# Performance work log

Measured on AMD Instinct MI355X. Metric: run time of the kernel, lower is better.

The kernel has to match this reference:

```python
import jax, jax.numpy as jnp
import numpy as np

H = 512          # hidden_size
SF = 4           # scale_factor
B, S, L = 16, 2048, 2

def setup_inputs() -> dict:
    key = jax.random.key(0)
    ks = jax.random.split(key, 9)
    return {
        "hidden": jax.random.normal(ks[0], (L, B, H * SF), dtype=jnp.float32),
        "encoder_outputs": jax.random.normal(ks[1], (B, S, H * SF), dtype=jnp.float32),
        "We": jax.random.normal(ks[2], (H, H * SF), dtype=jnp.float32) * 0.02,
        "be": jax.random.normal(ks[3], (H,), dtype=jnp.float32) * 0.02,
        "Wh": jax.random.normal(ks[4], (H, H * SF), dtype=jnp.float32) * 0.02,
        "bh": jax.random.normal(ks[5], (H,), dtype=jnp.float32) * 0.02,
        "Wa": jax.random.normal(ks[6], (H, 2 * H), dtype=jnp.float32) * 0.02,
        "ba": jax.random.normal(ks[7], (H,), dtype=jnp.float32) * 0.02,
        "v": jax.random.uniform(ks[8], (1, H), dtype=jnp.float32),
    }

def reference(hidden, encoder_outputs, We, be, Wh, bh, Wa, ba, v):
    # hidden[-1]: [B, 4H] -> [B, H]
    h = hidden[-1] @ Wh.T + bh
    # encoder_outputs: [B, S, 4H] -> [B, S, H]
    eo = jnp.einsum('bsf,hf->bsh', encoder_outputs, We) + be
    # concat([h broadcast to S, eo]) @ Wa.T == h @ Wa_h.T + eo @ Wa_e.T (split concat matmul)
    Wa_h, Wa_e = Wa[:, :H], Wa[:, H:]
    energy = jnp.tanh(h[:, None, :] @ Wa_h.T + jnp.einsum('bsh,kh->bsk', eo, Wa_e) + ba)  # [B,S,H]
    scores = jnp.einsum('bsh,h->bs', energy, v[0])           # [B,S]
    attn_weights = jax.nn.softmax(scores, axis=1)            # [B,S]
    context_vector = jnp.einsum('bs,bsh->bh', attn_weights, eo)  # [B,H]
    return (context_vector, attn_weights)
```

## Files before the change

kernel.cpp:

```cpp
#include <hip/hip_runtime.h>
#include <math.h>

#define HH 512
#define FF 2048
#define BB 16
#define SS 2048
#define MM 32768

using f32x4 = __attribute__((ext_vector_type(4))) float;
using s16x8 = __attribute__((ext_vector_type(8))) short;

struct __align__(8)  US4 { unsigned short x, y, z, w; };
struct __align__(16) US8 { unsigned short s[8]; };

__device__ __forceinline__ unsigned short f2bf(float f) {
  unsigned int u = __builtin_bit_cast(unsigned int, f);
  u += 0x7fffu + ((u >> 16) & 1u);
  return (unsigned short)(u >> 16);
}
__device__ __forceinline__ float bf2f(unsigned short u) {
  unsigned int x = ((unsigned int)u) << 16;
  return __builtin_bit_cast(float, x);
}
__device__ __forceinline__ void gload_lds16(const void* g, void* l) {
  __builtin_amdgcn_global_load_lds(
      (const __attribute__((address_space(1))) unsigned int*)g,
      (__attribute__((address_space(3))) unsigned int*)l, 16, 0, 0);
}

__global__ void k_conv(const float* __restrict__ We, const float* __restrict__ Wa,
                       unsigned short* __restrict__ OWe, unsigned short* __restrict__ OWa) {
  int bid = blockIdx.x, t = threadIdx.x;
  if (bid < 1024) {
    int idx = bid * 256 + t;
    f32x4 x = *(const f32x4*)(We + (size_t)idx * 4);
    US4 p{f2bf(x.x), f2bf(x.y), f2bf(x.z), f2bf(x.w)};
    *(US4*)(OWe + (size_t)idx * 4) = p;
  } else {
    int idx = (bid - 1024) * 256 + t;
    int k = idx >> 7, h4 = idx & 127;
    f32x4 x = *(const f32x4*)(Wa + (size_t)k * 1024 + 512 + h4 * 4);
    US4 p{f2bf(x.x), f2bf(x.y), f2bf(x.z), f2bf(x.w)};
    *(US4*)(OWa + (size_t)idx * 4) = p;
  }
}

__global__ void k_h(const float* __restrict__ hidden, const float* __restrict__ Wh,
                    const float* __restrict__ bh, float* __restrict__ h_ws) {
  int t = threadIdx.x, lane = t & 63, wid = t >> 6;
  int out = blockIdx.x * 4 + wid;
  int b = out >> 9, j = out & 511;
  const float* hr = hidden + (1) * BB * FF + b * FF;
  const float* wr = Wh + (size_t)j * FF;
  float a = 0.f;
#pragma unroll
  for (int i = 0; i < 8; ++i) {
    int o = i * 256 + lane * 4;
    f32x4 x = *(const f32x4*)(hr + o);
    f32x4 y = *(const f32x4*)(wr + o);
    a += x.x * y.x + x.y * y.y + x.z * y.z + x.w * y.w;
  }
#pragma unroll
  for (int m = 32; m; m >>= 1) a += __shfl_xor(a, m);
  if (lane == 0) h_ws[out] = a + bh[j];
}

__global__ void k_bb(const float* __restrict__ h_ws, const float* __restrict__ Wa,
                     const float* __restrict__ ba, float* __restrict__ bb_ws) {
  int t = threadIdx.x, lane = t & 63, wid = t >> 6;
  int out = blockIdx.x * 4 + wid;
  int b = out >> 9, k = out & 511;
  const float* hr = h_ws + b * HH;
  const float* wa = Wa + (size_t)k * 1024;
  float a = 0.f;
#pragma unroll
  for (int i = 0; i < 2; ++i) {
    int o = i * 256 + lane * 4;
    f32x4 x = *(const f32x4*)(hr + o);
    f32x4 y = *(const f32x4*)(wa + o);
    a += x.x * y.x + x.y * y.y + x.z * y.z + x.w * y.w;
  }
#pragma unroll
  for (int m = 32; m; m >>= 1) a += __shfl_xor(a, m);
  if (lane == 0) bb_ws[out] = a + ba[k];
}

__global__ __launch_bounds__(512, 4) void k_gemm1f(
    const float* __restrict__ enc, const unsigned short* __restrict__ Web,
    const float* __restrict__ be, const unsigned short* __restrict__ Waeb,
    const float* __restrict__ bbw, const float* __restrict__ vv,
    unsigned short* __restrict__ eo, float* __restrict__ sp) {
  __shared__ unsigned short smem[36864];
  unsigned short* As = smem;
  unsigned short* Bs = smem + 4096;
  const int t = threadIdx.x, lane = t & 63, wid = t >> 6;
  const int m0 = blockIdx.x * 64;
  const float* enc_m0 = enc + (size_t)m0 * FF;
  f32x4 acc[4][4] = {};

  f32x4 areg[2];
#pragma unroll
  for (int i = 0; i < 2; ++i) {
    int idx = i * 512 + t, row = idx >> 4, c4 = idx & 15;
    areg[i] = *(const f32x4*)(enc_m0 + (size_t)row * FF + c4 * 4);
  }

#pragma unroll 1
  for (int kt = 0; kt < FF; kt += 64) {
#pragma unroll
    for (int i = 0; i < 8; ++i) {
      int idx = i * 512 + t, row = idx >> 3, c = idx & 7, sc = c ^ (row & 7);
      gload_lds16(Web + (size_t)row * FF + kt + sc * 8, Bs + idx * 8);
    }
#pragma unroll
    for (int i = 0; i < 2; ++i) {
      int idx = i * 512 + t, row = idx >> 4, c4 = idx & 15;
      f32x4 x = areg[i];
      US4 p{f2bf(x.x), f2bf(x.y), f2bf(x.z), f2bf(x.w)};
      int byte = row * 128 + ((c4 * 8) ^ ((row & 7) << 4));
      *(US4*)((char*)As + byte) = p;
    }
    {
      int ktn = (kt + 64 < FF) ? kt + 64 : 0;
#pragma unroll
      for (int i = 0; i < 2; ++i) {
        int idx = i * 512 + t, row = idx >> 4, c4 = idx & 15;
        areg[i] = *(const f32x4*)(enc_m0 + (size_t)row * FF + ktn + c4 * 4);
      }
    }
    asm volatile("s_waitcnt vmcnt(2) lgkmcnt(0)" ::: "memory");
    __builtin_amdgcn_s_barrier();
    __builtin_amdgcn_sched_barrier(0);
#pragma unroll
    for (int ks = 0; ks < 2; ++ks) {
      s16x8 af[4], bfr[4];
#pragma unroll
      for (int mi = 0; mi < 4; ++mi) {
        int row = mi * 16 + (lane & 15);
        int byte = row * 128 + (((ks * 64) + (lane >> 4) * 16) ^ ((row & 7) << 4));
        af[mi] = *(const s16x8*)((const char*)As + byte);
      }
#pragma unroll
      for (int ni = 0; ni < 4; ++ni) {
        int row = wid * 64 + ni * 16 + (lane & 15);
        int byte = row * 128 + (((ks * 64) + (lane >> 4) * 16) ^ ((row & 7) << 4));
        bfr[ni] = *(const s16x8*)((const char*)Bs + byte);
      }
#pragma unroll
      for (int mi = 0; mi < 4; ++mi)
#pragma unroll
        for (int ni = 0; ni < 4; ++ni)
          acc[mi][ni] = __builtin_amdgcn_mfma_f32_16x16x32_bf16(af[mi], bfr[ni], acc[mi][ni], 0, 0, 0);
    }
    asm volatile("s_waitcnt lgkmcnt(0)" ::: "memory");
    __builtin_amdgcn_s_barrier();
    __builtin_amdgcn_sched_barrier(0);
  }

  unsigned short* Cs = smem + 4096;
#pragma unroll
  for (int ni = 0; ni < 4; ++ni) {
    int col = wid * 64 + ni * 16 + (lane & 15);
    float bev = be[col];
#pragma unroll
    for (int mi = 0; mi < 4; ++mi)
#pragma unroll
      for (int j = 0; j < 4; ++j) {
        int row = mi * 16 + (lane >> 4) * 4 + j;
        int byte = row * 1024 + ((col * 2) ^ ((row & 7) << 4));
        *(unsigned short*)((char*)Cs + byte) = f2bf(acc[mi][ni][j] + bev);
      }
  }
  __syncthreads();

#pragma unroll
  for (int i = 0; i < 8; ++i) {
    int idx = i * 512 + t, row = idx >> 6, c = idx & 63;
    int byte = row * 1024 + ((c * 16) ^ ((row & 7) << 4));
    *(US8*)(eo + (size_t)(m0 + row) * HH + c * 8) = *(const US8*)((const char*)Cs + byte);
  }

  f32x4 acc2[4][4] = {};
#pragma unroll
  for (int kt2 = 0; kt2 < HH; kt2 += 64) {
#pragma unroll
    for (int ks = 0; ks < 2; ++ks) {
      int k2 = kt2 + ks * 32 + (lane >> 4) * 8;
      s16x8 af[4], bfr[4];
#pragma unroll
      for (int mi = 0; mi < 4; ++mi) {
        int row = mi * 16 + (lane & 15);
        int byte = row * 1024 + ((k2 * 2) ^ ((row & 7) << 4));
        af[mi] = *(const s16x8*)((const char*)Cs + byte);
      }
#pragma unroll
      for (int ni = 0; ni < 4; ++ni) {
        int nrow = wid * 64 + ni * 16 + (lane & 15);
        bfr[ni] = *(const s16x8*)(Waeb + (size_t)nrow * HH + k2);
      }
#pragma unroll
      for (int mi = 0; mi < 4; ++mi)
#pragma unroll
        for (int ni = 0; ni < 4; ++ni)
          acc2[mi][ni] = __builtin_amdgcn_mfma_f32_16x16x32_bf16(af[mi], bfr[ni], acc2[mi][ni], 0, 0, 0);
    }
  }

  const int b = m0 >> 11;
  float vcol[4], bcol[4];
#pragma unroll
  for (int ni = 0; ni < 4; ++ni) {
    int col = wid * 64 + ni * 16 + (lane & 15);
    vcol[ni] = vv[col];
    bcol[ni] = bbw[b * HH + col];
  }
  float ps[4][4];
#pragma unroll
  for (int mi = 0; mi < 4; ++mi)
#pragma unroll
    for (int j = 0; j < 4; ++j) {
      float s = 0.f;
#pragma unroll
      for (int ni = 0; ni < 4; ++ni)
        s += tanhf(acc2[mi][ni][j] + bcol[ni]) * vcol[ni];
      ps[mi][j] = s;
    }
#pragma unroll
  for (int m = 1; m < 16; m <<= 1)
#pragma unroll
    for (int mi = 0; mi < 4; ++mi)
#pragma unroll
      for (int j = 0; j < 4; ++j) ps[mi][j] += __shfl_xor(ps[mi][j], m);
  float* red = (float*)smem;
  if ((lane & 15) == 0) {
#pragma unroll
    for (int mi = 0; mi < 4; ++mi)
#pragma unroll
      for (int j = 0; j < 4; ++j)
        red[wid * 64 + mi * 16 + (lane >> 4) * 4 + j] = ps[mi][j];
  }
  __syncthreads();
  if (t < 64) {
    float s = 0.f;
#pragma unroll
    for (int w = 0; w < 8; ++w) s += red[w * 64 + t];
    sp[m0 + t] = s;
  }
}

__global__ void k_softmax(const float* __restrict__ sp, float* __restrict__ attn) {
  const int b = blockIdx.x, t = threadIdx.x, lane = t & 63, wid = t >> 6;
  __shared__ float red[4];
  float vals[8], lmax = -3.0e38f;
#pragma unroll
  for (int i = 0; i < 8; ++i) {
    float x = sp[b * SS + t + i * 256];
    vals[i] = x;
    lmax = fmaxf(lmax, x);
  }
#pragma unroll
  for (int m = 32; m; m >>= 1) lmax = fmaxf(lmax, __shfl_xor(lmax, m));
  if (lane == 0) red[wid] = lmax;
  __syncthreads();
  lmax = fmaxf(fmaxf(red[0], red[1]), fmaxf(red[2], red[3]));
  __syncthreads();
  float lsum = 0.f;
#pragma unroll
  for (int i = 0; i < 8; ++i) {
    vals[i] = __expf(vals[i] - lmax);
    lsum += vals[i];
  }
#pragma unroll
  for (int m = 32; m; m >>= 1) lsum += __shfl_xor(lsum, m);
  if (lane == 0) red[wid] = lsum;
  __syncthreads();
  float inv = 1.0f / (red[0] + red[1] + red[2] + red[3]);
#pragma unroll
  for (int i = 0; i < 8; ++i) attn[b * SS + t + i * 256] = vals[i] * inv;
}

__global__ __launch_bounds__(512) void k_ctx1(const unsigned short* __restrict__ eo,
                                              const float* __restrict__ attn,
                                              float* __restrict__ cp) {
  __shared__ float red[8][512];
  const int b = blockIdx.x >> 4, ch = blockIdx.x & 15, t = threadIdx.x;
  const int tg = t & 63, sg = t >> 6;
  const float* aw = attn + b * SS + ch * 128;
  float acc[8] = {};
#pragma unroll 4
  for (int i = 0; i < 16; ++i) {
    int s = sg + i * 8;
    float w = aw[s];
    US8 vv8 = *(const US8*)(eo + (size_t)(b * SS + ch * 128 + s) * HH + tg * 8);
#pragma unroll
    for (int j = 0; j < 8; ++j) acc[j] += w * bf2f(vv8.s[j]);
  }
#pragma unroll
  for (int j = 0; j < 8; ++j) red[sg][tg * 8 + j] = acc[j];
  __syncthreads();
  float a = 0.f;
#pragma unroll
  for (int g = 0; g < 8; ++g) a += red[g][t];
  cp[(size_t)blockIdx.x * HH + t] = a;
}

__global__ void k_ctx2(const float* __restrict__ cp, float* __restrict__ ctx) {
  const int b = blockIdx.x, h = threadIdx.x;
  float a = 0.f;
#pragma unroll
  for (int c = 0; c < 16; ++c) a += cp[(size_t)(b * 16 + c) * HH + h];
  ctx[b * HH + h] = a;
}

extern "C" void kernel_launch(void* const* d_in, const int* in_sizes, int n_in,
                              void* d_out, int out_size, void* d_ws, size_t ws_size,
                              hipStream_t stream) {
  (void)in_sizes; (void)n_in; (void)out_size; (void)ws_size;
  const float* hidden = (const float*)d_in[0];
  const float* enc    = (const float*)d_in[1];
  const float* We     = (const float*)d_in[2];
  const float* be     = (const float*)d_in[3];
  const float* Wh     = (const float*)d_in[4];
  const float* bh     = (const float*)d_in[5];
  const float* Wa     = (const float*)d_in[6];
  const float* ba     = (const float*)d_in[7];
  const float* v      = (const float*)d_in[8];

  float* out  = (float*)d_out;
  float* ctx  = out;
  float* attn = out + BB * HH;

  char* ws = (char*)d_ws;
  unsigned short* Web  = (unsigned short*)ws;  ws += (size_t)HH * FF * 2;
  unsigned short* Waeb = (unsigned short*)ws;  ws += (size_t)HH * HH * 2;
  float* h_ws  = (float*)ws;                   ws += (size_t)BB * HH * 4;
  float* bb_ws = (float*)ws;                   ws += (size_t)BB * HH * 4;
  unsigned short* eo = (unsigned short*)ws;    ws += (size_t)MM * HH * 2;
  float* sp = (float*)ws;                      ws += (size_t)MM * 4;
  float* cp = (float*)ws;                      ws += (size_t)BB * 16 * HH * 4;

  k_conv<<<1280, 256, 0, stream>>>(We, Wa, Web, Waeb);
  k_h<<<2048, 256, 0, stream>>>(hidden, Wh, bh, h_ws);
  k_bb<<<2048, 256, 0, stream>>>(h_ws, Wa, ba, bb_ws);
  k_gemm1f<<<512, 512, 0, stream>>>(enc, Web, be, Waeb, bb_ws, v, eo, sp);
  k_softmax<<<16, 256, 0, stream>>>(sp, attn);
  k_ctx1<<<256, 512, 0, stream>>>(eo, attn, cp);
  k_ctx2<<<16, 512, 0, stream>>>(cp, ctx);
}
```

Measured before the change: 170.5 us.

## Load GEMM1 B fragments directly to registers and double-buffer A tile in LDS

The main encoder GEMM kernel no longer stages the bf16 weight tile through LDS with global_load_lds. Each wave now loads its B fragments straight from global memory into registers, ping-ponging between two register sets across the two k-halves. The fp32 activation tile is converted and written into a double-buffered LDS A tile, so each iteration needs one barrier and less LDS traffic. The cost is more VGPR pressure, uncoalesced per-lane global B loads that rely on L2 reuse across blocks, and a larger shared allocation that may lower occupancy.

```diff
diff --git a/kernel.cpp b/kernel.cpp
--- a/kernel.cpp
+++ b/kernel.cpp
@@ -21,11 +21,6 @@
 __device__ __forceinline__ float bf2f(unsigned short u) {
   unsigned int x = ((unsigned int)u) << 16;
   return __builtin_bit_cast(float, x);
-}
-__device__ __forceinline__ void gload_lds16(const void* g, void* l) {
-  __builtin_amdgcn_global_load_lds(
-      (const __attribute__((address_space(1))) unsigned int*)g,
-      (__attribute__((address_space(3))) unsigned int*)l, 16, 0, 0);
 }
 
 __global__ void k_conv(const float* __restrict__ We, const float* __restrict__ Wa,
@@ -90,74 +85,81 @@
     const float* __restrict__ be, const unsigned short* __restrict__ Waeb,
     const float* __restrict__ bbw, const float* __restrict__ vv,
     unsigned short* __restrict__ eo, float* __restrict__ sp) {
-  __shared__ unsigned short smem[36864];
-  unsigned short* As = smem;
-  unsigned short* Bs = smem + 4096;
+  __shared__ char smem[81920];
   const int t = threadIdx.x, lane = t & 63, wid = t >> 6;
   const int m0 = blockIdx.x * 64;
   const float* enc_m0 = enc + (size_t)m0 * FF;
   f32x4 acc[4][4] = {};
 
-  f32x4 areg[2];
-#pragma unroll
-  for (int i = 0; i < 2; ++i) {
-    int idx = i * 512 + t, row = idx >> 4, c4 = idx & 15;
-    areg[i] = *(const f32x4*)(enc_m0 + (size_t)row * FF + c4 * 4);
-  }
+  const int sRow = t & 63;
+  const int sKb  = t >> 6;
+  const int sDst = ((sKb * 4 + (sRow >> 4)) << 8) + ((sRow & 15) << 4);
+  const float* ap = enc_m0 + (size_t)sRow * FF + sKb * 8;
+
+  const unsigned short* bp = Web + (size_t)(wid * 64 + (lane & 15)) * FF + ((lane >> 4) << 3);
+
+  f32x4 ar0, ar1;
+  {
+    f32x4 w0 = *(const f32x4*)ap;
+    f32x4 w1 = *(const f32x4*)(ap + 4);
+    US8 o{f2bf(w0.x), f2bf(w0.y), f2bf(w0.z), f2bf(w0.w),
+          f2bf(w1.x), f2bf(w1.y), f2bf(w1.z), f2bf(w1.w)};
+    *(US8*)(smem + sDst) = o;
+    ar0 = *(const f32x4*)(ap + 64);
+    ar1 = *(const f32x4*)(ap + 68);
+  }
+  s16x8 bA[4], bB[4];
+#pragma unroll
+  for (int ni = 0; ni < 4; ++ni)
+    bA[ni] = *(const s16x8*)(bp + (size_t)ni * 16 * FF);
+  asm volatile("s_waitcnt lgkmcnt(0)" ::: "memory");
+  __builtin_amdgcn_s_barrier();
+  __builtin_amdgcn_sched_barrier(0);
 
 #pragma unroll 1
   for (int kt = 0; kt < FF; kt += 64) {
-#pragma unroll
-    for (int i = 0; i < 8; ++i) {
-      int idx = i * 512 + t, row = idx >> 3, c = idx & 7, sc = c ^ (row & 7);
-      gload_lds16(Web + (size_t)row * FF + kt + sc * 8, Bs + idx * 8);
-    }
-#pragma unroll
-    for (int i = 0; i < 2; ++i) {
-      int idx = i * 512 + t, row = idx >> 4, c4 = idx & 15;
-      f32x4 x = areg[i];
-      US4 p{f2bf(x.x), f2bf(x.y), f2bf(x.z), f2bf(x.w)};
-      int byte = row * 128 + ((c4 * 8) ^ ((row & 7) << 4));
-      *(US4*)((char*)As + byte) = p;
-    }
-    {
-      int ktn = (kt + 64 < FF) ? kt + 64 : 0;
-#pragma unroll
-      for (int i = 0; i < 2; ++i) {
-        int idx = i * 512 + t, row = idx >> 4, c4 = idx & 15;
-        areg[i] = *(const f32x4*)(enc_m0 + (size_t)row * FF + ktn + c4 * 4);
+    char* AsC = smem + (((kt >> 6) & 1) << 13);
+    char* AsN = smem + ((((kt >> 6) & 1) ^ 1) << 13);
+#pragma unroll
+    for (int ni = 0; ni < 4; ++ni)
+      bB[ni] = *(const s16x8*)(bp + (size_t)ni * 16 * FF + kt + 32);
+    if (kt < 1984) {
+      US8 o{f2bf(ar0.x), f2bf(ar0.y), f2bf(ar0.z), f2bf(ar0.w),
+            f2bf(ar1.x), f2bf(ar1.y), f2bf(ar1.z), f2bf(ar1.w)};
+      *(US8*)(AsN + sDst) = o;
+      if (kt < 1920) {
+        ar0 = *(const f32x4*)(ap + kt + 128);
+        ar1 = *(const f32x4*)(ap + kt + 132);
       }
     }
-    asm volatile("s_waitcnt vmcnt(2) lgkmcnt(0)" ::: "memory");
-    __builtin_amdgcn_s_barrier();
-    __builtin_amdgcn_sched_barrier(0);
-#pragma unroll
-    for (int ks = 0; ks < 2; ++ks) {
-      s16x8 af[4], bfr[4];
-#pragma unroll
-      for (int mi = 0; mi < 4; ++mi) {
-        int row = mi * 16 + (lane & 15);
-        int byte = row * 128 + (((ks * 64) + (lane >> 4) * 16) ^ ((row & 7) << 4));
-        af[mi] = *(const s16x8*)((const char*)As + byte);
-      }
-#pragma unroll
-      for (int ni = 0; ni < 4; ++ni) {
-        int row = wid * 64 + ni * 16 + (lane & 15);
-        int byte = row * 128 + (((ks * 64) + (lane >> 4) * 16) ^ ((row & 7) << 4));
-        bfr[ni] = *(const s16x8*)((const char*)Bs + byte);
-      }
-#pragma unroll
-      for (int mi = 0; mi < 4; ++mi)
-#pragma unroll
-        for (int ni = 0; ni < 4; ++ni)
-          acc[mi][ni] = __builtin_amdgcn_mfma_f32_16x16x32_bf16(af[mi], bfr[ni], acc[mi][ni], 0, 0, 0);
+    s16x8 af[4];
+#pragma unroll
+    for (int mi = 0; mi < 4; ++mi)
+      af[mi] = *(const s16x8*)(AsC + (((lane >> 4)) * 4 + mi) * 256 + ((lane & 15) << 4));
+#pragma unroll
+    for (int mi = 0; mi < 4; ++mi)
+#pragma unroll
+      for (int ni = 0; ni < 4; ++ni)
+        acc[mi][ni] = __builtin_amdgcn_mfma_f32_16x16x32_bf16(af[mi], bA[ni], acc[mi][ni], 0, 0, 0);
+    if (kt < 1984) {
+#pragma unroll
+      for (int ni = 0; ni < 4; ++ni)
+        bA[ni] = *(const s16x8*)(bp + (size_t)ni * 16 * FF + kt + 64);
     }
+#pragma unroll
+    for (int mi = 0; mi < 4; ++mi)
+      af[mi] = *(const s16x8*)(AsC + ((4 + (lane >> 4)) * 4 + mi) * 256 + ((lane & 15) << 4));
+#pragma unroll
+    for (int mi = 0; mi < 4; ++mi)
+#pragma unroll
+      for (int ni = 0; ni < 4; ++ni)
+        acc[mi][ni] = __builtin_amdgcn_mfma_f32_16x16x32_bf16(af[mi], bB[ni], acc[mi][ni], 0, 0, 0);
     asm volatile("s_waitcnt lgkmcnt(0)" ::: "memory");
     __builtin_amdgcn_s_barrier();
     __builtin_amdgcn_sched_barrier(0);
   }
 
-  unsigned short* Cs = smem + 4096;
+  unsigned short* Cs = (unsigned short*)(smem + 16384);
 #pragma unroll
   for (int ni = 0; ni < 4; ++ni) {
     int col = wid * 64 + ni * 16 + (lane & 15);
```

Result: slower. 243.7 us (+42.9%).

## Enlarge GEMM tile to 128 rows with double-buffered B in LDS

Applied to the files above, without the earlier changes.

The fused encoder GEMM kernel now processes 128 rows per block instead of 64. It double-buffers the We tile in LDS (a 144KB allocation) and lays A and B out in a fragment-friendly order without XOR swizzle. The K loop is unrolled two steps per iteration with register ping-pong for the fp32 A prefetch. The epilogue and second GEMM run in two 64-row halves. The aim is to halve the reloads of We per row of output and to overlap global loads with MFMA work, at the cost of one block per CU, only 256 blocks, and higher register pressure from 32 accumulators.

```diff
diff --git a/kernel.cpp b/kernel.cpp
--- a/kernel.cpp
+++ b/kernel.cpp
@@ -85,166 +85,215 @@
   if (lane == 0) bb_ws[out] = a + ba[k];
 }
 
-__global__ __launch_bounds__(512, 4) void k_gemm1f(
+template<int PAR, bool STB, bool LDA, bool WRA, int VM>
+__device__ __forceinline__ void stepB(
+    const float* apA, const float* apB, const unsigned short* Web, char* smem,
+    int kt, int t, int lane, int wid, int aDst0, int aDst1,
+    const int* bRow, const int* bKb,
+    f32x4& l0, f32x4& l1, f32x4& l2, f32x4& l3,
+    const f32x4& w0, const f32x4& w1, const f32x4& w2, const f32x4& w3,
+    f32x4 (&acc)[8][4]) {
+  char* BsC = smem + 16384 + (PAR << 16);
+  char* BsN = smem + 16384 + ((PAR ^ 1) << 16);
+  if (STB) {
+#pragma unroll
+    for (int i = 0; i < 8; ++i) {
+      int idx = i * 512 + t;
+      gload_lds16(Web + (size_t)bRow[i] * FF + (kt + 64) + bKb[i] * 8, BsN + idx * 16);
+    }
+  }
+  __builtin_amdgcn_sched_barrier(0);
+  if (LDA) {
+    l0 = *(const f32x4*)(apA + kt + 128);
+    l1 = *(const f32x4*)(apA + kt + 132);
+    l2 = *(const f32x4*)(apB + kt + 128);
+    l3 = *(const f32x4*)(apB + kt + 132);
+  }
+  __builtin_amdgcn_sched_barrier(0);
+#pragma unroll
+  for (int ks = 0; ks < 2; ++ks) {
+    s16x8 bfr[4];
+#pragma unroll
+    for (int ni = 0; ni < 4; ++ni)
+      bfr[ni] = *(const s16x8*)(BsC + ((ks * 4 + (lane >> 4)) * 32 + wid * 4 + ni) * 256 + ((lane & 15) << 4));
+#pragma unroll
+    for (int mi = 0; mi < 8; ++mi) {
+      s16x8 af = *(const s16x8*)(smem + ((ks * 4 + (lane >> 4)) * 8 + mi) * 256 + ((lane & 15) << 4));
+#pragma unroll
+      for (int ni = 0; ni < 4; ++ni)
+        acc[mi][ni] = __builtin_amdgcn_mfma_f32_16x16x32_bf16(af, bfr[ni], acc[mi][ni], 0, 0, 0);
+    }
+  }
+  asm volatile("s_waitcnt lgkmcnt(0)" ::: "memory");
+  __builtin_amdgcn_s_barrier();
+  __builtin_amdgcn_sched_barrier(0);
+  if (WRA) {
+    US8 oa{f2bf(w0.x), f2bf(w0.y), f2bf(w0.z), f2bf(w0.w),
+           f2bf(w1.x), f2bf(w1.y), f2bf(w1.z), f2bf(w1.w)};
+    *(US8*)(smem + aDst0) = oa;
+    US8 ob{f2bf(w2.x), f2bf(w2.y), f2bf(w2.z), f2bf(w2.w),
+           f2bf(w3.x), f2bf(w3.y), f2bf(w3.z), f2bf(w3.w)};
+    *(US8*)(smem + aDst1) = ob;
+  }
+  asm volatile("s_waitcnt vmcnt(%0) lgkmcnt(0)" :: "i"(VM) : "memory");
+  __builtin_amdgcn_s_barrier();
+  __builtin_amdgcn_sched_barrier(0);
+}
+
+__global__ __launch_bounds__(512, 2) void k_gemm1f(
     const float* __restrict__ enc, const unsigned short* __restrict__ Web,
     const float* __restrict__ be, const unsigned short* __restrict__ Waeb,
     const float* __restrict__ bbw, const float* __restrict__ vv,
     unsigned short* __restrict__ eo, float* __restrict__ sp) {
-  __shared__ unsigned short smem[36864];
-  unsigned short* As = smem;
-  unsigned short* Bs = smem + 4096;
+  __shared__ char smem[147456];
   const int t = threadIdx.x, lane = t & 63, wid = t >> 6;
-  const int m0 = blockIdx.x * 64;
+  const int m0 = blockIdx.x * 128;
   const float* enc_m0 = enc + (size_t)m0 * FF;
-  f32x4 acc[4][4] = {};
-
-  f32x4 areg[2];
-#pragma unroll
-  for (int i = 0; i < 2; ++i) {
-    int idx = i * 512 + t, row = idx >> 4, c4 = idx & 15;
-    areg[i] = *(const f32x4*)(enc_m0 + (size_t)row * FF + c4 * 4);
-  }
+  f32x4 acc[8][4] = {};
+
+  const int aRow = t & 127;
+  const int aKb0 = t >> 7;
+  const int aDst0 = ((aKb0 * 8 + (aRow >> 4)) << 8) + ((aRow & 15) << 4);
+  const int aDst1 = (((aKb0 + 4) * 8 + (aRow >> 4)) << 8) + ((aRow & 15) << 4);
+  const float* apA = enc_m0 + (size_t)aRow * FF + aKb0 * 8;
+  const float* apB = apA + 32;
+
+  int bRow[8], bKb[8];
+#pragma unroll
+  for (int i = 0; i < 8; ++i) {
+    int idx = i * 512 + t;
+    bRow[i] = ((idx >> 4) & 31) * 16 + (idx & 15);
+    bKb[i]  = idx >> 9;
+  }
+
+  f32x4 X0, X1, X2, X3, Y0, Y1, Y2, Y3;
+#pragma unroll
+  for (int i = 0; i < 8; ++i) {
+    int idx = i * 512 + t;
+    gload_lds16(Web + (size_t)bRow[i] * FF + bKb[i] * 8, smem + 16384 + idx * 16);
+  }
+  {
+    f32x4 a0 = *(const f32x4*)(apA);
+    f32x4 a1 = *(const f32x4*)(apA + 4);
+    f32x4 a2 = *(const f32x4*)(apB);
+    f32x4 a3 = *(const f32x4*)(apB + 4);
+    US8 oa{f2bf(a0.x), f2bf(a0.y), f2bf(a0.z), f2bf(a0.w),
+           f2bf(a1.x), f2bf(a1.y), f2bf(a1.z), f2bf(a1.w)};
+    *(US8*)(smem + aDst0) = oa;
+    US8 ob{f2bf(a2.x), f2bf(a2.y), f2bf(a2.z), f2bf(a2.w),
+           f2bf(a3.x), f2bf(a3.y), f2bf(a3.z), f2bf(a3.w)};
+    *(US8*)(smem + aDst1) = ob;
+    X0 = *(const f32x4*)(apA + 64);
+    X1 = *(const f32x4*)(apA + 68);
+    X2 = *(const f32x4*)(apB + 64);
+    X3 = *(const f32x4*)(apB + 68);
+  }
+  asm volatile("s_waitcnt vmcnt(0) lgkmcnt(0)" ::: "memory");
+  __builtin_amdgcn_s_barrier();
+  __builtin_amdgcn_sched_barrier(0);
 
 #pragma unroll 1
-  for (int kt = 0; kt < FF; kt += 64) {
+  for (int it = 0; it < 15; ++it) {
+    int kt = it << 7;
+    stepB<0, true, true, true, 4>(apA, apB, Web, smem, kt, t, lane, wid, aDst0, aDst1,
+                                  bRow, bKb, Y0, Y1, Y2, Y3, X0, X1, X2, X3, acc);
+    stepB<1, true, true, true, 4>(apA, apB, Web, smem, kt + 64, t, lane, wid, aDst0, aDst1,
+                                  bRow, bKb, X0, X1, X2, X3, Y0, Y1, Y2, Y3, acc);
+  }
+  stepB<0, true, false, true, 0>(apA, apB, Web, smem, 1920, t, lane, wid, aDst0, aDst1,
+                                 bRow, bKb, Y0, Y1, Y2, Y3, X0, X1, X2, X3, acc);
+  stepB<1, false, false, false, 0>(apA, apB, Web, smem, 1984, t, lane, wid, aDst0, aDst1,
+                                   bRow, bKb, X0, X1, X2, X3, Y0, Y1, Y2, Y3, acc);
+
+  unsigned short* Cs = (unsigned short*)(smem + 16384);
+  const int b = m0 >> 11;
+#pragma unroll 1
+  for (int h = 0; h < 2; ++h) {
+#pragma unroll
+    for (int ni = 0; ni < 4; ++ni) {
+      int col = wid * 64 + ni * 16 + (lane & 15);
+      float bev = be[col];
+#pragma unroll
+      for (int mi = 0; mi < 4; ++mi)
+#pragma unroll
+        for (int j = 0; j < 4; ++j) {
+          int row = mi * 16 + (lane >> 4) * 4 + j;
+          int byte = row * 1024 + ((col * 2) ^ ((row & 7) << 4));
+          *(unsigned short*)((char*)Cs + byte) = f2bf(acc[4 * h + mi][ni][j] + bev);
+        }
+    }
+    __syncthreads();
 #pragma unroll
     for (int i = 0; i < 8; ++i) {
-      int idx = i * 512 + t, row = idx >> 3, c = idx & 7, sc = c ^ (row & 7);
-      gload_lds16(Web + (size_t)row * FF + kt + sc * 8, Bs + idx * 8);
-    }
-#pragma unroll
-    for (int i = 0; i < 2; ++i) {
-      int idx = i * 512 + t, row = idx >> 4, c4 = idx & 15;
-      f32x4 x = areg[i];
-      US4 p{f2bf(x.x), f2bf(x.y), f2bf(x.z), f2bf(x.w)};
-      int byte = row * 128 + ((c4 * 8) ^ ((row & 7) << 4));
-      *(US4*)((char*)As + byte) = p;
-    }
-    {
-      int ktn = (kt + 64 < FF) ? kt + 64 : 0;
-#pragma unroll
-      for (int i = 0; i < 2; ++i) {
-        int idx = i * 512 + t, row = idx >> 4, c4 = idx & 15;
-        areg[i] = *(const f32x4*)(enc_m0 + (size_t)row * FF + ktn + c4 * 4);
+      int idx = i * 512 + t, row = idx >> 6, c = idx & 63;
+      int byte = row * 1024 + ((c * 16) ^ ((row & 7) << 4));
+      *(US8*)(eo + (size_t)(m0 + 64 * h + row) * HH + c * 8) = *(const US8*)((const char*)Cs + byte);
+    }
+    f32x4 acc2[4][4] = {};
+#pragma unroll
+    for (int kt2 = 0; kt2 < HH; kt2 += 64) {
+#pragma unroll
+      for (int ks = 0; ks < 2; ++ks) {
+        int k2 = kt2 + ks * 32 + (lane >> 4) * 8;
+        s16x8 af[4], bfr[4];
+#pragma unroll
+        for (int mi = 0; mi < 4; ++mi) {
+          int row = mi * 16 + (lane & 15);
+          int byte = row * 1024 + ((k2 * 2) ^ ((row & 7) << 4));
+          af[mi] = *(const s16x8*)((const char*)Cs + byte);
+        }
+#pragma unroll
+        for (int ni = 0; ni < 4; ++ni) {
+          int nrow = wid * 64 + ni * 16 + (lane & 15);
+          bfr[ni] = *(const s16x8*)(Waeb + (size_t)nrow * HH + k2);
+        }
+#pragma unroll
+        for (int mi = 0; mi < 4; ++mi)
+#pragma unroll
+          for (int ni = 0; ni < 4; ++ni)
+            acc2[mi][ni] = __builtin_amdgcn_mfma_f32_16x16x32_bf16(af[mi], bfr[ni], acc2[mi][ni], 0, 0, 0);
       }
     }
-    asm volatile("s_waitcnt vmcnt(2) lgkmcnt(0)" ::: "memory");
-    __builtin_amdgcn_s_barrier();
-    __builtin_amdgcn_sched_barrier(0);
-#pragma unroll
-    for (int ks = 0; ks < 2; ++ks) {
-      s16x8 af[4], bfr[4];
-#pragma unroll
-      for (int mi = 0; mi < 4; ++mi) {
-        int row = mi * 16 + (lane & 15);
-        int byte = row * 128 + (((ks * 64) + (lane >> 4) * 16) ^ ((row & 7) << 4));
-        af[mi] = *(const s16x8*)((const char*)As + byte);
+    float vcol[4], bcol[4];
+#pragma unroll
+    for (int ni = 0; ni < 4; ++ni) {
+      int col = wid * 64 + ni * 16 + (lane & 15);
+      vcol[ni] = vv[col];
+      bcol[ni] = bbw[b * HH + col];
+    }
+    float ps[4][4];
+#pragma unroll
+    for (int mi = 0; mi < 4; ++mi)
+#pragma unroll
+      for (int j = 0; j < 4; ++j) {
+        float s = 0.f;
+#pragma unroll
+        for (int ni = 0; ni < 4; ++ni)
+          s += tanhf(acc2[mi][ni][j] + bcol[ni]) * vcol[ni];
+        ps[mi][j] = s;
       }
 #pragma unroll
-      for (int ni = 0; ni < 4; ++ni) {
-        int row = wid * 64 + ni * 16 + (lane & 15);
-        int byte = row * 128 + (((ks * 64) + (lane >> 4) * 16) ^ ((row & 7) << 4));
-        bfr[ni] = *(const s16x8*)((const char*)Bs + byte);
-      }
+    for (int m = 1; m < 16; m <<= 1)
 #pragma unroll
       for (int mi = 0; mi < 4; ++mi)
 #pragma unroll
-        for (int ni = 0; ni < 4; ++ni)
-          acc[mi][ni] = __builtin_amdgcn_mfma_f32_16x16x32_bf16(af[mi], bfr[ni], acc[mi][ni], 0, 0, 0);
-    }
-    asm volatile("s_waitcnt lgkmcnt(0)" ::: "memory");
-    __builtin_amdgcn_s_barrier();
-    __builtin_amdgcn_sched_barrier(0);
-  }
-
-  unsigned short* Cs = smem + 4096;
-#pragma unroll
-  for (int ni = 0; ni < 4; ++ni) {
-    int col = wid * 64 + ni * 16 + (lane & 15);
-    float bev = be[col];
-#pragma unroll
-    for (int mi = 0; mi < 4; ++mi)
-#pragma unroll
-      for (int j = 0; j < 4; ++j) {
-        int row = mi * 16 + (lane >> 4) * 4 + j;
-        int byte = row * 1024 + ((col * 2) ^ ((row & 7) << 4));
-        *(unsigned short*)((char*)Cs + byte) = f2bf(acc[mi][ni][j] + bev);
-      }
-  }
-  __syncthreads();
-
-#pragma unroll
-  for (int i = 0; i < 8; ++i) {
-    int idx = i * 512 + t, row = idx >> 6, c = idx & 63;
-    int byte = row * 1024 + ((c * 16) ^ ((row & 7) << 4));
-    *(US8*)(eo + (size_t)(m0 + row) * HH + c * 8) = *(const US8*)((const char*)Cs + byte);
-  }
-
-  f32x4 acc2[4][4] = {};
-#pragma unroll
-  for (int kt2 = 0; kt2 < HH; kt2 += 64) {
-#pragma unroll
-    for (int ks = 0; ks < 2; ++ks) {
-      int k2 = kt2 + ks * 32 + (lane >> 4) * 8;
-      s16x8 af[4], bfr[4];
-#pragma unroll
-      for (int mi = 0; mi < 4; ++mi) {
-        int row = mi * 16 + (lane & 15);
-        int byte = row * 1024 + ((k2 * 2) ^ ((row & 7) << 4));
-        af[mi] = *(const s16x8*)((const char*)Cs + byte);
-      }
-#pragma unroll
-      for (int ni = 0; ni < 4; ++ni) {
-        int nrow = wid * 64 + ni * 16 + (lane & 15);
-        bfr[ni] = *(const s16x8*)(Waeb + (size_t)nrow * HH + k2);
-      }
+        for (int j = 0; j < 4; ++j) ps[mi][j] += __shfl_xor(ps[mi][j], m);
+    float* red = (float*)smem;
+    if ((lane & 15) == 0) {
 #pragma unroll
       for (int mi = 0; mi < 4; ++mi)
 #pragma unroll
-        for (int ni = 0; ni < 4; ++ni)
-          acc2[mi][ni] = __builtin_amdgcn_mfma_f32_16x16x32_bf16(af[mi], bfr[ni], acc2[mi][ni], 0, 0, 0);
-    }
-  }
-
-  const int b = m0 >> 11;
-  float vcol[4], bcol[4];
-#pragma unroll
-  for (int ni = 0; ni < 4; ++ni) {
-    int col = wid * 64 + ni * 16 + (lane & 15);
-    vcol[ni] = vv[col];
-    bcol[ni] = bbw[b * HH + col];
-  }
-  float ps[4][4];
-#pragma unroll
-  for (int mi = 0; mi < 4; ++mi)
-#pragma unroll
-    for (int j = 0; j < 4; ++j) {
+        for (int j = 0; j < 4; ++j)
+          red[wid * 64 + mi * 16 + (lane >> 4) * 4 + j] = ps[mi][j];
+    }
+    __syncthreads();
+    if (t < 64) {
       float s = 0.f;
 #pragma unroll
-      for (int ni = 0; ni < 4; ++ni)
-        s += tanhf(acc2[mi][ni][j] + bcol[ni]) * vcol[ni];
-      ps[mi][j] = s;
-    }
-#pragma unroll
-  for (int m = 1; m < 16; m <<= 1)
-#pragma unroll
-    for (int mi = 0; mi < 4; ++mi)
-#pragma unroll
-      for (int j = 0; j < 4; ++j) ps[mi][j] += __shfl_xor(ps[mi][j], m);
-  float* red = (float*)smem;
-  if ((lane & 15) == 0) {
-#pragma unroll
-    for (int mi = 0; mi < 4; ++mi)
-#pragma unroll
-      for (int j = 0; j < 4; ++j)
-        red[wid * 64 + mi * 16 + (lane >> 4) * 4 + j] = ps[mi][j];
-  }
-  __syncthreads();
-  if (t < 64) {
-    float s = 0.f;
-#pragma unroll
-    for (int w = 0; w < 8; ++w) s += red[w * 64 + t];
-    sp[m0 + t] = s;
+      for (int w = 0; w < 8; ++w) s += red[w * 64 + t];
+      sp[m0 + 64 * h + t] = s;
+    }
+    __syncthreads();
   }
 }
 
@@ -342,7 +391,7 @@
   k_conv<<<1280, 256, 0, stream>>>(We, Wa, Web, Waeb);
   k_h<<<2048, 256, 0, stream>>>(hidden, Wh, bh, h_ws);
   k_bb<<<2048, 256, 0, stream>>>(h_ws, Wa, ba, bb_ws);
-  k_gemm1f<<<512, 512, 0, stream>>>(enc, Web, be, Waeb, bb_ws, v, eo, sp);
+  k_gemm1f<<<256, 512, 0, stream>>>(enc, Web, be, Waeb, bb_ws, v, eo, sp);
   k_softmax<<<16, 256, 0, stream>>>(sp, attn);
   k_ctx1<<<256, 512, 0, stream>>>(eo, attn, cp);
   k_ctx2<<<16, 512, 0, stream>>>(cp, ctx);
```

Result: slower. 393.2 us (+130.6%).
